# Kernel optimization log

Measured on AMD Instinct MI355X. Metric: run time of the kernel, lower is better.

Reference implementation:

```python
import jax, jax.numpy as jnp
import numpy as np

NUM_HEADS = 16
LN_EPS = 1e-5


def _rope(x):
    """lucidrains RotaryEmbedding(dim_per_head // 2): rotate only the first
    Dh//2 channels with interleaved pairs; pass the rest through.
    x: (B, H, S, Dh)"""
    S, D = x.shape[-2], x.shape[-1]
    rot = D // 2
    inv_freq = 1.0 / (10000.0 ** (jnp.arange(0, rot, 2, dtype=jnp.float32) / rot))  # (rot//2,)
    ang = jnp.arange(S, dtype=jnp.float32)[:, None] * inv_freq[None, :]             # (S, rot//2)
    ang = jnp.repeat(ang, 2, axis=-1)                                               # (S, rot)
    cos, sin = jnp.cos(ang), jnp.sin(ang)
    xr, xp = x[..., :rot], x[..., rot:]
    x1, x2 = xr[..., 0::2], xr[..., 1::2]
    rot_half = jnp.stack((-x2, x1), axis=-1).reshape(xr.shape)  # interleaved (-x2, x1)
    xr = xr * cos + rot_half * sin
    return jnp.concatenate([xr, xp], axis=-1)


def setup_inputs() -> dict:
    key = jax.random.key(0)
    k1, k2, k3 = jax.random.split(key, 3)
    B, S, D = 4, 2048, 2048
    X = jax.random.normal(k1, (B, S, D), dtype=jnp.float32)
    ln_w = jnp.ones((D,), dtype=jnp.float32)
    ln_b = jnp.zeros((D,), dtype=jnp.float32)
    W_in = jax.random.normal(k2, (D, 3 * D), dtype=jnp.float32) * 0.02
    W_out = jax.random.normal(k3, (D, D), dtype=jnp.float32) * 0.02
    return {"X": X, "ln_w": ln_w, "ln_b": ln_b, "W_in": W_in, "W_out": W_out}


def reference(X, ln_w, ln_b, W_in, W_out):
    B, S, D = X.shape
    H = NUM_HEADS
    Dh = D // H
    # pre-norm (LayerNorm)
    mu = jnp.mean(X, axis=-1, keepdims=True)
    var = jnp.mean(jnp.square(X - mu), axis=-1, keepdims=True)
    Xn = (X - mu) * jax.lax.rsqrt(var + LN_EPS) * ln_w + ln_b
    # fused QKV projection
    qkv = jnp.einsum('bsd,df->bsf', Xn, W_in)            # (B, S, 3D)
    Q, K, V = jnp.split(qkv, 3, axis=-1)
    Q = Q.reshape(B, S, H, Dh).transpose(0, 2, 1, 3)     # (B, H, S, Dh)
    K = K.reshape(B, S, H, Dh).transpose(0, 2, 1, 3)
    V = V.reshape(B, S, H, Dh).transpose(0, 2, 1, 3)
    Q, K = _rope(Q), _rope(K)
    scores = jnp.einsum('bhqd,bhkd->bhqk', Q, K) / jnp.sqrt(jnp.float32(Dh))
    probs = jax.nn.softmax(scores, axis=-1)              # acausal: no mask
    ctx = jnp.einsum('bhqk,bhkd->bhqd', probs, V)
    ctx = ctx.transpose(0, 2, 1, 3).reshape(B, S, D)
    out = jnp.einsum('bsd,df->bsf', ctx, W_out)
    return out + X
```

## Files before the change

kernel.cpp:

```cpp
#include <hip/hip_runtime.h>
#include <hip/hip_bf16.h>
#include <cstddef>

#define B_ 4
#define S_ 2048
#define D_ 2048
#define H_ 16
#define DH_ 128
#define QKS_ 4096
#define BS_ 8192

typedef __attribute__((ext_vector_type(8))) short bfrag8;
typedef __attribute__((ext_vector_type(4))) float ffrag4;

typedef const __attribute__((address_space(1))) void* gptr1;
typedef __attribute__((address_space(3))) void* lptr3;
#define GL16(g, l) __builtin_amdgcn_global_load_lds((gptr1)(g), (lptr3)(l), 16, 0, 0)

__device__ __forceinline__ short f2bf(float f) {
  unsigned u = __float_as_uint(f);
  u = (u + 0x7FFFu + ((u >> 16) & 1u)) >> 16;
  return (short)u;
}
__device__ __forceinline__ float bf2f(short s) {
  return __uint_as_float(((unsigned)(unsigned short)s) << 16);
}
__device__ __forceinline__ unsigned pk2(float lo, float hi) {
  unsigned a = __float_as_uint(lo);
  a = (a + 0x7FFFu + ((a >> 16) & 1u)) >> 16;
  unsigned b = __float_as_uint(hi);
  b = (b + 0x7FFFu + ((b >> 16) & 1u)) & 0xFFFF0000u;
  return a | b;
}

__global__ __launch_bounds__(256) void rope_tab_kernel(float2* __restrict__ tab) {
  int idx = blockIdx.x * 256 + threadIdx.x;
  int s = idx >> 5, p = idx & 31;
  float invf = exp2f(-(float)p * (13.287712379549449f / 32.0f));
  float sn, cs;
  sincosf((float)s * invf, &sn, &cs);
  tab[idx] = make_float2(cs, sn);
}

__global__ __launch_bounds__(256) void ln_kernel(const float* __restrict__ X,
    const float* __restrict__ w, const float* __restrict__ bta,
    short* __restrict__ Xn) {
  int row = blockIdx.x;
  int tid = threadIdx.x;
  const float* xr = X + (size_t)row * D_;
  float x[8];
  float4 v0 = *(const float4*)(xr + tid * 4);
  float4 v1 = *(const float4*)(xr + 1024 + tid * 4);
  x[0] = v0.x; x[1] = v0.y; x[2] = v0.z; x[3] = v0.w;
  x[4] = v1.x; x[5] = v1.y; x[6] = v1.z; x[7] = v1.w;
  float sum = 0.f, ssq = 0.f;
#pragma unroll
  for (int i = 0; i < 8; i++) { sum += x[i]; ssq += x[i] * x[i]; }
#pragma unroll
  for (int off = 1; off < 64; off <<= 1) {
    sum += __shfl_xor(sum, off, 64);
    ssq += __shfl_xor(ssq, off, 64);
  }
  __shared__ float s1[4], s2[4];
  int wave = tid >> 6;
  if ((tid & 63) == 0) { s1[wave] = sum; s2[wave] = ssq; }
  __syncthreads();
  sum = s1[0] + s1[1] + s1[2] + s1[3];
  ssq = s2[0] + s2[1] + s2[2] + s2[3];
  float mu = sum * (1.0f / D_);
  float var = ssq * (1.0f / D_) - mu * mu;
  float rs = rsqrtf(var + 1e-5f);
  short* orow = Xn + (size_t)row * D_;
#pragma unroll
  for (int i = 0; i < 8; i++) {
    int col = (i < 4) ? (tid * 4 + i) : (1024 + tid * 4 + (i - 4));
    float xn = (x[i] - mu) * rs * w[col] + bta[col];
    orow[col] = f2bf(xn);
  }
}

__global__ __launch_bounds__(256) void transpose_cvt(const float* __restrict__ W,
    short* __restrict__ WT, int R, int C) {
  __shared__ float t[32][33];
  int tx = threadIdx.x, ty = threadIdx.y;
  int c0 = blockIdx.x * 32, r0 = blockIdx.y * 32;
#pragma unroll
  for (int i = 0; i < 4; i++)
    t[ty + i * 8][tx] = W[(size_t)(r0 + ty + i * 8) * C + c0 + tx];
  __syncthreads();
#pragma unroll
  for (int i = 0; i < 4; i++)
    WT[(size_t)(c0 + ty + i * 8) * R + r0 + tx] = f2bf(t[tx][ty + i * 8]);
}

template<int EPI>
__global__ __launch_bounds__(256) void gemm_bt(const short* __restrict__ A,
    const short* __restrict__ Bt, short* __restrict__ Cb, short* __restrict__ Vt,
    const float2* __restrict__ tab, float* __restrict__ Cf,
    const float* __restrict__ resid, int M, int N, int K) {
  __shared__ __align__(16) short lA[128 * 64];
  __shared__ __align__(16) short lB[128 * 64];
  int tid = threadIdx.x;
  int m0 = blockIdx.y * 128, n0 = blockIdx.x * 128;
  int wave = tid >> 6, lane = tid & 63;
  int m16 = lane & 15, quad = lane >> 4;
  int wm = (wave >> 1) * 64, wn = (wave & 1) * 64;
  const ffrag4 fzero = {0.f, 0.f, 0.f, 0.f};
  ffrag4 acc[4][4];
#pragma unroll
  for (int i = 0; i < 4; i++)
#pragma unroll
    for (int j = 0; j < 4; j++) acc[i][j] = fzero;

  int srow = lane >> 3;
  int scb  = lane & 7;
  for (int k0 = 0; k0 < K; k0 += 64) {
#pragma unroll
    for (int i = 0; i < 4; i++) {
      int c = i * 4 + wave;
      int r = c * 8 + srow;
      int sb = scb ^ (r & 7);
      GL16(A + (size_t)(m0 + r) * K + k0 + sb * 8, lA + c * 512);
      GL16(Bt + (size_t)(n0 + r) * K + k0 + sb * 8, lB + c * 512);
    }
    __syncthreads();
#pragma unroll
    for (int kk = 0; kk < 2; kk++) {
      bfrag8 af[4], bfb[4];
#pragma unroll
      for (int t = 0; t < 4; t++) {
        int ra = wm + t * 16 + m16;
        int rb = wn + t * 16 + m16;
        int blk = kk * 4 + quad;
        af[t] = *(const bfrag8*)(lA + ra * 64 + ((blk ^ (ra & 7)) << 3));
        bfb[t] = *(const bfrag8*)(lB + rb * 64 + ((blk ^ (rb & 7)) << 3));
      }
#pragma unroll
      for (int i = 0; i < 4; i++)
#pragma unroll
        for (int j = 0; j < 4; j++)
          acc[i][j] = __builtin_amdgcn_mfma_f32_16x16x32_bf16(af[i], bfb[j], acc[i][j], 0, 0, 0);
    }
    __syncthreads();
  }

#pragma unroll
  for (int i = 0; i < 4; i++) {
    int rowb = m0 + wm + i * 16 + quad * 4;
#pragma unroll
    for (int j = 0; j < 4; j++) {
      int col = n0 + wn + j * 16 + m16;
      if (EPI == 1) {
#pragma unroll
        for (int r = 0; r < 4; r++) {
          size_t idx = (size_t)(rowb + r) * N + col;
          Cf[idx] = acc[i][j][r] + resid[idx];
        }
      } else if (n0 >= 4096) {
        int d = col - 4096;
        short4 pk;
        pk.x = f2bf(acc[i][j][0]);
        pk.y = f2bf(acc[i][j][1]);
        pk.z = f2bf(acc[i][j][2]);
        pk.w = f2bf(acc[i][j][3]);
        *(short4*)(Vt + ((size_t)((rowb >> 11) * H_ + (d >> 7)) * DH_ + (d & 127)) * S_ +
                   (rowb & (S_ - 1))) = pk;
      } else if ((col & 127) < 64) {
        int p = (col & 127) >> 1;
        float sgn = (col & 1) ? 1.0f : -1.0f;
#pragma unroll
        for (int r = 0; r < 4; r++) {
          float own = acc[i][j][r];
          float prt = __shfl_xor(own, 1, 64);
          float2 cssn = tab[((rowb + r) & (S_ - 1)) * 32 + p];
          Cb[(size_t)(rowb + r) * QKS_ + col] = f2bf(own * cssn.x + sgn * prt * cssn.y);
        }
      } else {
#pragma unroll
        for (int r = 0; r < 4; r++)
          Cb[(size_t)(rowb + r) * QKS_ + col] = f2bf(acc[i][j][r]);
      }
    }
  }
}

__global__ __launch_bounds__(512) void attn_kernel(const short* __restrict__ qkv,
    const short* __restrict__ Vt, short* __restrict__ ctx) {
  __shared__ __align__(16) short lK[2][64 * 128];
  __shared__ __align__(16) short lV[2][128 * 64];
  int tid = threadIdx.x;
  int wave = tid >> 6, lane = tid & 63;
  int m16 = lane & 15, quad = lane >> 4;
  int bh = blockIdx.y;
  int b = bh >> 4, h = bh & 15;
  int qbase = blockIdx.x * 256 + wave * 32;

  const float qscale = 1.4426950408889634f * 0.08838834764831845f;
  bfrag8 qf[2][4];
#pragma unroll
  for (int qb = 0; qb < 2; qb++)
#pragma unroll
    for (int kc = 0; kc < 4; kc++) {
      bfrag8 q = *(const bfrag8*)(qkv +
          (size_t)(b * S_ + qbase + qb * 16 + m16) * QKS_ + h * DH_ + kc * 32 + quad * 8);
#pragma unroll
      for (int j = 0; j < 8; j++) q[j] = f2bf(bf2f(q[j]) * qscale);
      qf[qb][kc] = q;
    }

  const ffrag4 fzero = {0.f, 0.f, 0.f, 0.f};
  ffrag4 oacc[2][8];
#pragma unroll
  for (int qb = 0; qb < 2; qb++)
#pragma unroll
    for (int nd = 0; nd < 8; nd++) oacc[qb][nd] = fzero;
  float lpart[2] = {0.f, 0.f};

  int krow = lane >> 4;
  int kcb = lane & 15;
  int vrow = lane >> 3;
  int vcb = lane & 7;

  {
#pragma unroll
    for (int i = 0; i < 2; i++) {
      int c = wave + i * 8;
      int r = c * 4 + krow;
      int sb = kcb ^ (r & 15);
      GL16(qkv + (size_t)(b * S_ + r) * QKS_ + D_ + h * DH_ + sb * 8, &lK[0][c * 512]);
    }
#pragma unroll
    for (int i = 0; i < 2; i++) {
      int c = wave + i * 8;
      int r = c * 8 + vrow;
      int sb = vcb ^ (r & 7);
      GL16(Vt + (size_t)(bh * DH_ + r) * S_ + sb * 8, &lV[0][c * 512]);
    }
  }
  __syncthreads();

  for (int kt = 0; kt < 32; kt++) {
    int cur = kt & 1;
    if (kt < 31) {
      int sk0 = (kt + 1) * 64;
      int nb = cur ^ 1;
#pragma unroll
      for (int i = 0; i < 2; i++) {
        int c = wave + i * 8;
        int r = c * 4 + krow;
        int sb = kcb ^ (r & 15);
        GL16(qkv + (size_t)(b * S_ + sk0 + r) * QKS_ + D_ + h * DH_ + sb * 8, &lK[nb][c * 512]);
      }
#pragma unroll
      for (int i = 0; i < 2; i++) {
        int c = wave + i * 8;
        int r = c * 8 + vrow;
        int sb = vcb ^ (r & 7);
        GL16(Vt + (size_t)(bh * DH_ + r) * S_ + sk0 + sb * 8, &lV[nb][c * 512]);
      }
    }

    const short* kb = &lK[cur][0];
    const short* vb = &lV[cur][0];

    ffrag4 sacc[2][4];
#pragma unroll
    for (int qb = 0; qb < 2; qb++)
#pragma unroll
      for (int ntk = 0; ntk < 4; ntk++) sacc[qb][ntk] = fzero;
#pragma unroll
    for (int ntk = 0; ntk < 4; ntk++)
#pragma unroll
      for (int kc = 0; kc < 4; kc++) {
        bfrag8 kf = *(const bfrag8*)(kb + (ntk * 16 + m16) * 128 +
                                     (((kc * 4 + quad) ^ m16) << 3));
        sacc[0][ntk] = __builtin_amdgcn_mfma_f32_16x16x32_bf16(kf, qf[0][kc], sacc[0][ntk], 0, 0, 0);
        sacc[1][ntk] = __builtin_amdgcn_mfma_f32_16x16x32_bf16(kf, qf[1][kc], sacc[1][ntk], 0, 0, 0);
      }

    bfrag8 pA[2][2];
#pragma unroll
    for (int qb = 0; qb < 2; qb++) {
      unsigned Xp[4][2];
      float ls = 0.f;
#pragma unroll
      for (int ntk = 0; ntk < 4; ntk++) {
        float e0 = exp2f(sacc[qb][ntk][0]);
        float e1 = exp2f(sacc[qb][ntk][1]);
        float e2 = exp2f(sacc[qb][ntk][2]);
        float e3 = exp2f(sacc[qb][ntk][3]);
        ls += (e0 + e1) + (e2 + e3);
        Xp[ntk][0] = pk2(e0, e1);
        Xp[ntk][1] = pk2(e2, e3);
      }
      lpart[qb] += ls;
#pragma unroll
      for (int kc = 0; kc < 2; kc++) {
        unsigned x0 = Xp[2 * kc][0], x1 = Xp[2 * kc][1];
        unsigned y0 = Xp[2 * kc + 1][0], y1 = Xp[2 * kc + 1][1];
        asm("v_permlane32_swap_b32 %0, %1" : "+v"(x0), "+v"(y0));
        asm("v_permlane16_swap_b32 %0, %1" : "+v"(x0), "+v"(y0));
        asm("v_permlane32_swap_b32 %0, %1" : "+v"(x1), "+v"(y1));
        asm("v_permlane16_swap_b32 %0, %1" : "+v"(x1), "+v"(y1));
        union { int4 i4; bfrag8 b8; } u;
        u.i4 = (int4){(int)x0, (int)x1, (int)y0, (int)y1};
        pA[qb][kc] = u.b8;
      }
    }

#pragma unroll
    for (int kc = 0; kc < 2; kc++)
#pragma unroll
      for (int nd = 0; nd < 8; nd++) {
        bfrag8 vf = *(const bfrag8*)(vb + (nd * 16 + m16) * 64 +
                                     (((kc * 4 + quad) ^ (m16 & 7)) << 3));
        oacc[0][nd] = __builtin_amdgcn_mfma_f32_16x16x32_bf16(pA[0][kc], vf, oacc[0][nd], 0, 0, 0);
        oacc[1][nd] = __builtin_amdgcn_mfma_f32_16x16x32_bf16(pA[1][kc], vf, oacc[1][nd], 0, 0, 0);
      }

    __syncthreads();
  }

#pragma unroll
  for (int qb = 0; qb < 2; qb++) {
    lpart[qb] += __shfl_xor(lpart[qb], 16, 64);
    lpart[qb] += __shfl_xor(lpart[qb], 32, 64);
  }
#pragma unroll
  for (int qb = 0; qb < 2; qb++) {
    float inv[4];
#pragma unroll
    for (int r = 0; r < 4; r++) inv[r] = 1.0f / __shfl(lpart[qb], quad * 4 + r, 64);
#pragma unroll
    for (int nd = 0; nd < 8; nd++)
#pragma unroll
      for (int r = 0; r < 4; r++) {
        int row = qbase + qb * 16 + quad * 4 + r;
        int col = h * DH_ + nd * 16 + m16;
        ctx[(size_t)(b * S_ + row) * D_ + col] = f2bf(oacc[qb][nd][r] * inv[r]);
      }
  }
}

extern "C" void kernel_launch(void* const* d_in, const int* in_sizes, int n_in,
                              void* d_out, int out_size, void* d_ws, size_t ws_size,
                              hipStream_t stream) {
  const float* X    = (const float*)d_in[0];
  const float* lnw  = (const float*)d_in[1];
  const float* lnb  = (const float*)d_in[2];
  const float* Win  = (const float*)d_in[3];
  const float* Wout = (const float*)d_in[4];
  float* out = (float*)d_out;
  char* ws = (char*)d_ws;
  short*  Xn    = (short*)(ws + 0);
  short*  WinT  = (short*)(ws + 33554432);
  short*  WoutT = (short*)(ws + 58720256);
  short*  qkv   = (short*)(ws + 67108864);
  short*  Vt    = (short*)(ws + 134217728);
  short*  ctx   = (short*)(ws + 167772160);
  float2* tab   = (float2*)(ws + 201326592);

  rope_tab_kernel<<<256, 256, 0, stream>>>(tab);
  transpose_cvt<<<dim3(192, 64), dim3(32, 8), 0, stream>>>(Win, WinT, 2048, 6144);
  transpose_cvt<<<dim3(64, 64), dim3(32, 8), 0, stream>>>(Wout, WoutT, 2048, 2048);
  ln_kernel<<<8192, 256, 0, stream>>>(X, lnw, lnb, Xn);
  gemm_bt<0><<<dim3(48, 64), 256, 0, stream>>>(Xn, WinT, qkv, Vt, tab, nullptr, nullptr, 8192, 6144, 2048);
  attn_kernel<<<dim3(8, 64), 512, 0, stream>>>(qkv, Vt, ctx);
  gemm_bt<1><<<dim3(16, 64), 256, 0, stream>>>(ctx, WoutT, nullptr, nullptr, nullptr, out, X, 8192, 2048, 2048);
}
```

Measured before the change: 715.7 us.

## Rewrite GEMM as 256x256 tile, 8-wave, double-buffered async-LDS pipeline

Replaces the 128x128, 4-wave GEMM that synchronises twice per step with a 256x256 tile computed by 8 waves. The K dimension is split into half-tiles that are double-buffered, and global-to-LDS loads are issued between MFMA phases with explicit vmcnt waits and raw barriers. MFMA sections are wrapped in s_setprio. The goal is to overlap memory transfers with matrix math and raise data reuse per tile, cutting stalls in the two projection GEMMs. In exchange, per-thread accumulator registers double (128 floats) and the grid shrinks to 768 and 256 blocks, which may leave the output-projection GEMM with poor CU occupancy.

Result: faster. 683.7 us (-4.5%).

```diff
diff --git a/kernel.cpp b/kernel.cpp
--- a/kernel.cpp
+++ b/kernel.cpp
@@ -8,7 +8,6 @@
 #define H_ 16
 #define DH_ 128
 #define QKS_ 4096
-#define BS_ 8192
 
 typedef __attribute__((ext_vector_type(8))) short bfrag8;
 typedef __attribute__((ext_vector_type(4))) float ffrag4;
@@ -16,6 +15,11 @@
 typedef const __attribute__((address_space(1))) void* gptr1;
 typedef __attribute__((address_space(3))) void* lptr3;
 #define GL16(g, l) __builtin_amdgcn_global_load_lds((gptr1)(g), (lptr3)(l), 16, 0, 0)
+
+#define BARRIER() { asm volatile("" ::: "memory"); __builtin_amdgcn_s_barrier(); asm volatile("" ::: "memory"); }
+#define VMW8() asm volatile("s_waitcnt vmcnt(8)" ::: "memory")
+#define VMW4() asm volatile("s_waitcnt vmcnt(4)" ::: "memory")
+#define VMW0() asm volatile("s_waitcnt vmcnt(0)" ::: "memory")
 
 __device__ __forceinline__ short f2bf(float f) {
   unsigned u = __float_as_uint(f);
@@ -94,75 +98,145 @@
 }
 
 template<int EPI>
-__global__ __launch_bounds__(256) void gemm_bt(const short* __restrict__ A,
+__global__ __launch_bounds__(512) void gemm_bt(const short* __restrict__ A,
     const short* __restrict__ Bt, short* __restrict__ Cb, short* __restrict__ Vt,
     const float2* __restrict__ tab, float* __restrict__ Cf,
     const float* __restrict__ resid, int M, int N, int K) {
-  __shared__ __align__(16) short lA[128 * 64];
-  __shared__ __align__(16) short lB[128 * 64];
+  __shared__ __align__(16) short lA[2][2][256][32];
+  __shared__ __align__(16) short lB[2][2][256][32];
   int tid = threadIdx.x;
-  int m0 = blockIdx.y * 128, n0 = blockIdx.x * 128;
   int wave = tid >> 6, lane = tid & 63;
   int m16 = lane & 15, quad = lane >> 4;
-  int wm = (wave >> 1) * 64, wn = (wave & 1) * 64;
+  int wm = (wave >> 2) * 128, wn = (wave & 3) * 64;
+  int m0 = blockIdx.y * 256, n0 = blockIdx.x * 256;
+
   const ffrag4 fzero = {0.f, 0.f, 0.f, 0.f};
-  ffrag4 acc[4][4];
-#pragma unroll
-  for (int i = 0; i < 4; i++)
+  ffrag4 acc[8][4];
+#pragma unroll
+  for (int i = 0; i < 8; i++)
 #pragma unroll
     for (int j = 0; j < 4; j++) acc[i][j] = fzero;
 
-  int srow = lane >> 3;
-  int scb  = lane & 7;
-  for (int k0 = 0; k0 < K; k0 += 64) {
-#pragma unroll
-    for (int i = 0; i < 4; i++) {
-      int c = i * 4 + wave;
-      int r = c * 8 + srow;
-      int sb = scb ^ (r & 7);
-      GL16(A + (size_t)(m0 + r) * K + k0 + sb * 8, lA + c * 512);
-      GL16(Bt + (size_t)(n0 + r) * K + k0 + sb * 8, lB + c * 512);
-    }
-    __syncthreads();
-#pragma unroll
-    for (int kk = 0; kk < 2; kk++) {
-      bfrag8 af[4], bfb[4];
-#pragma unroll
-      for (int t = 0; t < 4; t++) {
-        int ra = wm + t * 16 + m16;
-        int rb = wn + t * 16 + m16;
-        int blk = kk * 4 + quad;
-        af[t] = *(const bfrag8*)(lA + ra * 64 + ((blk ^ (ra & 7)) << 3));
-        bfb[t] = *(const bfrag8*)(lB + rb * 64 + ((blk ^ (rb & 7)) << 3));
-      }
-#pragma unroll
-      for (int i = 0; i < 4; i++)
-#pragma unroll
-        for (int j = 0; j < 4; j++)
-          acc[i][j] = __builtin_amdgcn_mfma_f32_16x16x32_bf16(af[i], bfb[j], acc[i][j], 0, 0, 0);
-    }
-    __syncthreads();
-  }
-
-#pragma unroll
-  for (int i = 0; i < 4; i++) {
-    int rowb = m0 + wm + i * 16 + quad * 4;
-#pragma unroll
-    for (int j = 0; j < 4; j++) {
-      int col = n0 + wn + j * 16 + m16;
+  const short* Abase = A + (size_t)m0 * K;
+  const short* Bbase = Bt + (size_t)n0 * K;
+
+#define STG(arr, gb, kt, h, d) { \
+    { int r_ = tid >> 2; int c_ = (tid & 3) ^ (r_ & 3); \
+      GL16((gb) + (size_t)r_ * K + (size_t)(kt) * 64 + (h) * 32 + c_ * 8, \
+           &(arr)[d][h][0][0] + (wave * 64) * 8); } \
+    { int r_ = (512 + tid) >> 2; int c_ = (tid & 3) ^ (r_ & 3); \
+      GL16((gb) + (size_t)r_ * K + (size_t)(kt) * 64 + (h) * 32 + c_ * 8, \
+           &(arr)[d][h][0][0] + ((512 + wave * 64)) * 8); } }
+
+  STG(lA, Abase, 0, 0, 0); STG(lB, Bbase, 0, 0, 0);
+  STG(lA, Abase, 0, 1, 0); STG(lB, Bbase, 0, 1, 0);
+  STG(lA, Abase, 1, 0, 1); STG(lB, Bbase, 1, 0, 1);
+  VMW8();
+  BARRIER();
+
+  int nK = K >> 6;
+  for (int t = 0; t < nK; ++t) {
+    int cur = t & 1, nxt = cur ^ 1;
+    int s1 = (t + 1 < nK), s2 = (t + 2 < nK);
+    bfrag8 bf[4], af[4];
+
+#pragma unroll
+    for (int ni = 0; ni < 4; ni++) {
+      int rb = wn + ni * 16 + m16;
+      bf[ni] = *(const bfrag8*)(&lB[cur][0][rb][(quad ^ (rb & 3)) << 3]);
+    }
+#pragma unroll
+    for (int mi = 0; mi < 4; mi++) {
+      int ra = wm + mi * 16 + m16;
+      af[mi] = *(const bfrag8*)(&lA[cur][0][ra][(quad ^ (ra & 3)) << 3]);
+    }
+    if (s1) STG(lA, Abase, t + 1, 1, nxt);
+    BARRIER();
+    __builtin_amdgcn_s_setprio(1);
+#pragma unroll
+    for (int mi = 0; mi < 4; mi++)
+#pragma unroll
+      for (int ni = 0; ni < 4; ni++)
+        acc[mi][ni] = __builtin_amdgcn_mfma_f32_16x16x32_bf16(af[mi], bf[ni], acc[mi][ni], 0, 0, 0);
+    __builtin_amdgcn_s_setprio(0);
+    BARRIER();
+
+#pragma unroll
+    for (int mi = 0; mi < 4; mi++) {
+      int ra = wm + (mi + 4) * 16 + m16;
+      af[mi] = *(const bfrag8*)(&lA[cur][0][ra][(quad ^ (ra & 3)) << 3]);
+    }
+    if (s1) STG(lB, Bbase, t + 1, 1, nxt);
+    BARRIER();
+    __builtin_amdgcn_s_setprio(1);
+#pragma unroll
+    for (int mi = 0; mi < 4; mi++)
+#pragma unroll
+      for (int ni = 0; ni < 4; ni++)
+        acc[mi + 4][ni] = __builtin_amdgcn_mfma_f32_16x16x32_bf16(af[mi], bf[ni], acc[mi + 4][ni], 0, 0, 0);
+    __builtin_amdgcn_s_setprio(0);
+    if (s1) { VMW8(); } else { VMW0(); }
+    BARRIER();
+
+#pragma unroll
+    for (int ni = 0; ni < 4; ni++) {
+      int rb = wn + ni * 16 + m16;
+      bf[ni] = *(const bfrag8*)(&lB[cur][1][rb][(quad ^ (rb & 3)) << 3]);
+    }
+#pragma unroll
+    for (int mi = 0; mi < 4; mi++) {
+      int ra = wm + mi * 16 + m16;
+      af[mi] = *(const bfrag8*)(&lA[cur][1][ra][(quad ^ (ra & 3)) << 3]);
+    }
+    if (s2) STG(lA, Abase, t + 2, 0, cur);
+    BARRIER();
+    __builtin_amdgcn_s_setprio(1);
+#pragma unroll
+    for (int mi = 0; mi < 4; mi++)
+#pragma unroll
+      for (int ni = 0; ni < 4; ni++)
+        acc[mi][ni] = __builtin_amdgcn_mfma_f32_16x16x32_bf16(af[mi], bf[ni], acc[mi][ni], 0, 0, 0);
+    __builtin_amdgcn_s_setprio(0);
+    BARRIER();
+
+#pragma unroll
+    for (int mi = 0; mi < 4; mi++) {
+      int ra = wm + (mi + 4) * 16 + m16;
+      af[mi] = *(const bfrag8*)(&lA[cur][1][ra][(quad ^ (ra & 3)) << 3]);
+    }
+    if (s2) STG(lB, Bbase, t + 2, 0, cur);
+    BARRIER();
+    __builtin_amdgcn_s_setprio(1);
+#pragma unroll
+    for (int mi = 0; mi < 4; mi++)
+#pragma unroll
+      for (int ni = 0; ni < 4; ni++)
+        acc[mi + 4][ni] = __builtin_amdgcn_mfma_f32_16x16x32_bf16(af[mi], bf[ni], acc[mi + 4][ni], 0, 0, 0);
+    __builtin_amdgcn_s_setprio(0);
+    if (s2) { VMW8(); } else if (s1) { VMW4(); }
+    BARRIER();
+  }
+#undef STG
+
+#pragma unroll
+  for (int mi = 0; mi < 8; mi++) {
+    int rowb = m0 + wm + mi * 16 + quad * 4;
+#pragma unroll
+    for (int ni = 0; ni < 4; ni++) {
+      int col = n0 + wn + ni * 16 + m16;
       if (EPI == 1) {
 #pragma unroll
         for (int r = 0; r < 4; r++) {
           size_t idx = (size_t)(rowb + r) * N + col;
-          Cf[idx] = acc[i][j][r] + resid[idx];
+          Cf[idx] = acc[mi][ni][r] + resid[idx];
         }
       } else if (n0 >= 4096) {
         int d = col - 4096;
         short4 pk;
-        pk.x = f2bf(acc[i][j][0]);
-        pk.y = f2bf(acc[i][j][1]);
-        pk.z = f2bf(acc[i][j][2]);
-        pk.w = f2bf(acc[i][j][3]);
+        pk.x = f2bf(acc[mi][ni][0]);
+        pk.y = f2bf(acc[mi][ni][1]);
+        pk.z = f2bf(acc[mi][ni][2]);
+        pk.w = f2bf(acc[mi][ni][3]);
         *(short4*)(Vt + ((size_t)((rowb >> 11) * H_ + (d >> 7)) * DH_ + (d & 127)) * S_ +
                    (rowb & (S_ - 1))) = pk;
       } else if ((col & 127) < 64) {
@@ -170,7 +244,7 @@
         float sgn = (col & 1) ? 1.0f : -1.0f;
 #pragma unroll
         for (int r = 0; r < 4; r++) {
-          float own = acc[i][j][r];
+          float own = acc[mi][ni][r];
           float prt = __shfl_xor(own, 1, 64);
           float2 cssn = tab[((rowb + r) & (S_ - 1)) * 32 + p];
           Cb[(size_t)(rowb + r) * QKS_ + col] = f2bf(own * cssn.x + sgn * prt * cssn.y);
@@ -178,7 +252,7 @@
       } else {
 #pragma unroll
         for (int r = 0; r < 4; r++)
-          Cb[(size_t)(rowb + r) * QKS_ + col] = f2bf(acc[i][j][r]);
+          Cb[(size_t)(rowb + r) * QKS_ + col] = f2bf(acc[mi][ni][r]);
       }
     }
   }
@@ -364,7 +438,7 @@
   transpose_cvt<<<dim3(192, 64), dim3(32, 8), 0, stream>>>(Win, WinT, 2048, 6144);
   transpose_cvt<<<dim3(64, 64), dim3(32, 8), 0, stream>>>(Wout, WoutT, 2048, 2048);
   ln_kernel<<<8192, 256, 0, stream>>>(X, lnw, lnb, Xn);
-  gemm_bt<0><<<dim3(48, 64), 256, 0, stream>>>(Xn, WinT, qkv, Vt, tab, nullptr, nullptr, 8192, 6144, 2048);
+  gemm_bt<0><<<dim3(24, 32), 512, 0, stream>>>(Xn, WinT, qkv, Vt, tab, nullptr, nullptr, 8192, 6144, 2048);
   attn_kernel<<<dim3(8, 64), 512, 0, stream>>>(qkv, Vt, ctx);
-  gemm_bt<1><<<dim3(16, 64), 256, 0, stream>>>(ctx, WoutT, nullptr, nullptr, nullptr, out, X, 8192, 2048, 2048);
-}
+  gemm_bt<1><<<dim3(8, 32), 512, 0, stream>>>(ctx, WoutT, nullptr, nullptr, nullptr, out, X, 8192, 2048, 2048);
+}
```
